# Performance work log

Hardware: AMD Instinct MI355X
Metric: run time of the kernel (lower is better)

## Reference

```python
import jax, jax.numpy as jnp
import numpy as np

HEADS = 12
DIM_HEAD = 64
SCALE = DIM_HEAD ** -0.5


def setup_inputs() -> dict:
    key = jax.random.key(0)
    k1, k2, k3 = jax.random.split(key, 3)
    B, N, D = 4, 2048, 768
    inner = HEADS * DIM_HEAD  # 768
    x = jax.random.normal(k1, (B, N, D), dtype=jnp.float32)
    W_qkv = jax.random.normal(k2, (D, 3 * inner), dtype=jnp.float32) * (D ** -0.5)
    W_out = jax.random.normal(k3, (inner, D), dtype=jnp.float32) * (inner ** -0.5)
    b_out = jnp.zeros((D,), dtype=jnp.float32)
    return {"x": x, "W_qkv": W_qkv, "W_out": W_out, "b_out": b_out}


def reference(x, W_qkv, W_out, b_out):
    B, N, D = x.shape
    qkv = x @ W_qkv  # [B, N, 3*inner]
    q, k, v = jnp.split(qkv, 3, axis=-1)
    # 'b n (h d) -> b h n d'
    def split_heads(t):
        return t.reshape(B, N, HEADS, DIM_HEAD).transpose(0, 2, 1, 3)
    q, k, v = split_heads(q), split_heads(k), split_heads(v)
    dots = jnp.einsum('bhnd,bhmd->bhnm', q, k) * SCALE  # [B, H, N, N]
    attn = jax.nn.softmax(dots, axis=-1)
    out = jnp.einsum('bhnm,bhmd->bhnd', attn, v)
    out = out.transpose(0, 2, 1, 3).reshape(B, N, HEADS * DIM_HEAD)  # 'b h n d -> b n (h d)'
    return out @ W_out + b_out
```

## Files before the change

kernel.cpp:

```cpp
#include <hip/hip_runtime.h>
#include <hip/hip_bf16.h>

typedef __bf16 bf16_t;
typedef __bf16 bf16x4 __attribute__((ext_vector_type(4)));
typedef __bf16 bf16x8 __attribute__((ext_vector_type(8)));
typedef float f32x4 __attribute__((ext_vector_type(4)));
typedef float f32x16 __attribute__((ext_vector_type(16)));
typedef unsigned int u32x4 __attribute__((ext_vector_type(4)));

#define HEADS 12
#define DHEAD 64
#define NSEQ 2048
#define BATCH 4
#define DMODEL 768
#define NINNER 768

#define QSCALE 0.18033688011112042f

__device__ __forceinline__ void gl_lds16(const bf16_t* g, bf16_t* l) {
  __builtin_amdgcn_global_load_lds(
      (const __attribute__((address_space(1))) void*)g,
      (__attribute__((address_space(3))) void*)l, 16, 0, 0);
}

__device__ __forceinline__ unsigned pack_bf16_2(float a, float b) {
  unsigned lo = (unsigned)__builtin_bit_cast(unsigned short, (bf16_t)a);
  unsigned hi = (unsigned)__builtin_bit_cast(unsigned short, (bf16_t)b);
  return lo | (hi << 16);
}

__global__ void cast_bf16_kernel(const float* __restrict__ in, bf16_t* __restrict__ out, int n8) {
  int i = blockIdx.x * blockDim.x + threadIdx.x;
  const int stride = gridDim.x * blockDim.x;
  for (; i < n8; i += stride) {
    const f32x4* p = (const f32x4*)(in + (size_t)i * 8);
    f32x4 a = p[0], b = p[1];
    bf16x8 o;
#pragma unroll
    for (int j = 0; j < 4; ++j) { o[j] = (bf16_t)a[j]; o[j + 4] = (bf16_t)b[j]; }
    *(bf16x8*)(out + (size_t)i * 8) = o;
  }
}

__global__ void transpose_cast_kernel(const float* __restrict__ in, bf16_t* __restrict__ out,
                                      int K, int N) {
  __shared__ float tile[32][33];
  const int bx = blockIdx.x * 32;
  const int by = blockIdx.y * 32;
  const int tx = threadIdx.x, ty = threadIdx.y;
#pragma unroll
  for (int i = ty; i < 32; i += 8)
    tile[i][tx] = in[(size_t)(by + i) * N + bx + tx];
  __syncthreads();
#pragma unroll
  for (int i = ty; i < 32; i += 8)
    out[(size_t)(bx + i) * K + by + tx] = (bf16_t)tile[tx][i];
}

template <int MODE>
__global__ __launch_bounds__(256, 2)
void gemm_bt(const bf16_t* __restrict__ A, const bf16_t* __restrict__ Bt,
             bf16_t* __restrict__ qw, bf16_t* __restrict__ kw, bf16_t* __restrict__ vtw,
             const float* __restrict__ bias, float* __restrict__ outf,
             int M, int Nn, int K) {
  __shared__ bf16_t As[128 * 64];
  __shared__ bf16_t Bs[128 * 64];
  const int tid = threadIdx.x;
  const int wid = tid >> 6;
  const int lane = tid & 63;
  const int m0 = blockIdx.x * 128;
  const int n0 = blockIdx.y * 128;
  const int arow = lane >> 3;
  const int acol = (lane & 7) * 8;
  const int wm = (wid >> 1) * 64;
  const int wn = (wid & 1) * 64;
  const int fr = lane & 15;
  const int fg = lane >> 4;

  f32x4 acc[4][4] = {};

  for (int kt = 0; kt < K; kt += 64) {
    __syncthreads();
#pragma unroll
    for (int i = 0; i < 4; ++i) {
      const int c = i * 4 + wid;
      gl_lds16(A + (size_t)(m0 + c * 8 + arow) * K + kt + acol, As + c * 512);
      gl_lds16(Bt + (size_t)(n0 + c * 8 + arow) * K + kt + acol, Bs + c * 512);
    }
    __syncthreads();
#pragma unroll
    for (int kk = 0; kk < 2; ++kk) {
      bf16x8 af[4], bfr[4];
#pragma unroll
      for (int mi = 0; mi < 4; ++mi)
        af[mi] = *(const bf16x8*)(As + (wm + mi * 16 + fr) * 64 + kk * 32 + fg * 8);
#pragma unroll
      for (int ni = 0; ni < 4; ++ni)
        bfr[ni] = *(const bf16x8*)(Bs + (wn + ni * 16 + fr) * 64 + kk * 32 + fg * 8);
#pragma unroll
      for (int mi = 0; mi < 4; ++mi)
#pragma unroll
        for (int ni = 0; ni < 4; ++ni)
          acc[mi][ni] = __builtin_amdgcn_mfma_f32_16x16x32_bf16(af[mi], bfr[ni], acc[mi][ni], 0, 0, 0);
    }
  }

  if (MODE == 0 && n0 >= 2 * NINNER) {
#pragma unroll
    for (int mi = 0; mi < 4; ++mi) {
#pragma unroll
      for (int ni = 0; ni < 4; ++ni) {
        const int col = n0 + wn + ni * 16 + fr - 2 * NINNER;
        const int h = col >> 6, d = col & 63;
        const int row0 = m0 + wm + mi * 16 + fg * 4;
        const int b = row0 >> 11, n = row0 & 2047;
        bf16x4 pk;
#pragma unroll
        for (int r = 0; r < 4; ++r) pk[r] = (bf16_t)acc[mi][ni][r];
        *(bf16x4*)(vtw + ((size_t)((b * HEADS + h) * DHEAD + d)) * NSEQ + n) = pk;
      }
    }
  } else {
#pragma unroll
    for (int mi = 0; mi < 4; ++mi) {
#pragma unroll
      for (int ni = 0; ni < 4; ++ni) {
#pragma unroll
        for (int r = 0; r < 4; ++r) {
          const int row = m0 + wm + mi * 16 + fg * 4 + r;
          const int col = n0 + wn + ni * 16 + fr;
          float val = acc[mi][ni][r];
          if (MODE == 0) {
            const int which = col / NINNER;
            const int cin = col - which * NINNER;
            const int h = cin >> 6, d = cin & 63;
            const int b = row >> 11, n = row & 2047;
            bf16_t* dst = (which == 0) ? qw : kw;
            if (which == 0) val *= QSCALE;
            dst[(((size_t)(b * HEADS + h)) * NSEQ + n) * DHEAD + d] = (bf16_t)val;
          } else {
            outf[(size_t)row * Nn + col] = val + bias[col];
          }
        }
      }
    }
  }
}

__global__ __launch_bounds__(256, 3)
void attn_fwd(const bf16_t* __restrict__ qg, const bf16_t* __restrict__ kg,
              const bf16_t* __restrict__ vtg, bf16_t* __restrict__ og) {
  __shared__ bf16_t KV[2][16 * 512];
  const int tid = threadIdx.x, wid = tid >> 6, lane = tid & 63;
  const int logical = (blockIdx.x & 7) * 96 + (blockIdx.x >> 3);
  const int bh = logical >> 4;
  const int qbase = (logical & 15) * 128 + wid * 32;
  const bf16_t* Q = qg + (size_t)bh * NSEQ * DHEAD;
  const bf16_t* K = kg + (size_t)bh * NSEQ * DHEAD;
  const bf16_t* Vt = vtg + (size_t)bh * NSEQ * DHEAD;
  const int l31 = lane & 31, hi = lane >> 5;
  const int sw = (l31 & 19) | ((l31 & 4) << 1) | ((l31 & 8) >> 1);

  bf16x8 qf[4];
#pragma unroll
  for (int ks = 0; ks < 4; ++ks)
    qf[ks] = *(const bf16x8*)(Q + (size_t)(qbase + l31) * DHEAD + ks * 16 + hi * 8);

  bf16x8 onesf;
#pragma unroll
  for (int e = 0; e < 8; ++e) onesf[e] = (bf16_t)1.0f;

  f32x16 oacc[2] = {};
  f32x16 lacc = {};

  auto stage = [&](int bsel, int t) {
    const int kv0 = t * 64;
#pragma unroll
    for (int i = 0; i < 4; ++i) {
      const int c = wid * 4 + i;
      bf16_t* dst = &KV[bsel][c * 512];
      if (c < 8) {
        gl_lds16(K + (size_t)(kv0 + (c >> 2) * 32 + sw) * DHEAD + (c & 3) * 16 + hi * 8, dst);
      } else {
        gl_lds16(Vt + (size_t)(((c >> 2) & 1) * 32 + l31) * NSEQ + kv0 + (c & 3) * 16 + hi * 8, dst);
      }
    }
  };

  stage(0, 0);

  for (int t = 0; t < NSEQ / 64; ++t) {
    const int buf = t & 1;
    asm volatile("s_waitcnt vmcnt(0) lgkmcnt(0)" ::: "memory");
    __builtin_amdgcn_sched_barrier(0);
    __syncthreads();
    if (t + 1 < NSEQ / 64) stage(buf ^ 1, t + 1);

    const bf16_t* base = &KV[buf][0];

    f32x16 sacc[2] = {};
    __builtin_amdgcn_s_setprio(1);
#pragma unroll
    for (int mi = 0; mi < 2; ++mi)
#pragma unroll
      for (int ks = 0; ks < 4; ++ks) {
        bf16x8 kf = *(const bf16x8*)(base + (mi * 4 + ks) * 512 + lane * 8);
        sacc[mi] = __builtin_amdgcn_mfma_f32_32x32x16_bf16(kf, qf[ks], sacc[mi], 0, 0, 0);
      }
    __builtin_amdgcn_s_setprio(0);

    bf16x8 pa[4];
#pragma unroll
    for (int mi = 0; mi < 2; ++mi) {
      float p[16];
#pragma unroll
      for (int r = 0; r < 16; ++r) p[r] = __builtin_amdgcn_exp2f(sacc[mi][r]);
#pragma unroll
      for (int s = 0; s < 2; ++s) {
        u32x4 pw;
#pragma unroll
        for (int w = 0; w < 4; ++w)
          pw[w] = pack_bf16_2(p[8 * s + 2 * w], p[8 * s + 2 * w + 1]);
        pa[mi * 2 + s] = __builtin_bit_cast(bf16x8, pw);
      }
    }

    __builtin_amdgcn_s_setprio(1);
#pragma unroll
    for (int ni = 0; ni < 2; ++ni)
#pragma unroll
      for (int ks = 0; ks < 4; ++ks) {
        bf16x8 vf = *(const bf16x8*)(base + (8 + ni * 4 + ks) * 512 + lane * 8);
        oacc[ni] = __builtin_amdgcn_mfma_f32_32x32x16_bf16(pa[ks], vf, oacc[ni], 0, 0, 0);
      }
#pragma unroll
    for (int ks = 0; ks < 4; ++ks)
      lacc = __builtin_amdgcn_mfma_f32_32x32x16_bf16(pa[ks], onesf, lacc, 0, 0, 0);
    __builtin_amdgcn_s_setprio(0);
  }

  const int b = bh / HEADS, h = bh % HEADS;
#pragma unroll
  for (int r = 0; r < 16; ++r) {
    const int qq = (r & 3) + 8 * (r >> 2) + 4 * hi;
    const float invr = 1.0f / lacc[r];
    const int n = qbase + qq;
#pragma unroll
    for (int ni = 0; ni < 2; ++ni)
      og[((size_t)b * NSEQ + n) * DMODEL + h * DHEAD + ni * 32 + l31] =
          (bf16_t)(oacc[ni][r] * invr);
  }
}

extern "C" void kernel_launch(void* const* d_in, const int* in_sizes, int n_in,
                              void* d_out, int out_size, void* d_ws, size_t ws_size,
                              hipStream_t stream) {
  const float* x    = (const float*)d_in[0];
  const float* Wqkv = (const float*)d_in[1];
  const float* Wout = (const float*)d_in[2];
  const float* bout = (const float*)d_in[3];
  float* out = (float*)d_out;

  char* ws = (char*)d_ws;
  bf16_t* xb    = (bf16_t*)(ws + 0);
  bf16_t* wqkvT = (bf16_t*)(ws + 12582912);
  bf16_t* woutT = (bf16_t*)(ws + 16121856);
  bf16_t* qw    = (bf16_t*)(ws + 17301504);
  bf16_t* kw    = (bf16_t*)(ws + 29884416);
  bf16_t* vtw   = (bf16_t*)(ws + 42467328);
  bf16_t* attno = (bf16_t*)(ws + 55050240);

  cast_bf16_kernel<<<1024, 256, 0, stream>>>(x, xb, (8192 * 768) / 8);
  transpose_cast_kernel<<<dim3(2304 / 32, 768 / 32), dim3(32, 8), 0, stream>>>(Wqkv, wqkvT, 768, 2304);
  transpose_cast_kernel<<<dim3(768 / 32, 768 / 32), dim3(32, 8), 0, stream>>>(Wout, woutT, 768, 768);

  gemm_bt<0><<<dim3(64, 18), 256, 0, stream>>>(xb, wqkvT, qw, kw, vtw, nullptr, nullptr,
                                               8192, 2304, 768);
  attn_fwd<<<768, 256, 0, stream>>>(qw, kw, vtw, attno);
  gemm_bt<1><<<dim3(64, 6), 256, 0, stream>>>(attno, woutT, nullptr, nullptr, nullptr, bout, out,
                                              8192, 768, 768);
}
```

Before: 151.6 us.

## Double-buffer GEMM LDS tiles and swizzle block order across XCDs

The GEMM kernels now use two LDS buffers, so the global-to-LDS load for the next K tile is issued before the MFMA work on the current tile. This is meant to hide load latency behind compute. The launch also changes to a 1D grid whose block index is remapped in groups of eight, spreading neighbouring tiles across XCDs for better L2 reuse. LDS use doubles to 64KB per block, which may limit occupancy. There is still a full wait and barrier on every iteration.

```diff
diff --git a/kernel.cpp b/kernel.cpp
--- a/kernel.cpp
+++ b/kernel.cpp
@@ -63,13 +63,16 @@
              bf16_t* __restrict__ qw, bf16_t* __restrict__ kw, bf16_t* __restrict__ vtw,
              const float* __restrict__ bias, float* __restrict__ outf,
              int M, int Nn, int K) {
-  __shared__ bf16_t As[128 * 64];
-  __shared__ bf16_t Bs[128 * 64];
+  __shared__ bf16_t As[2][128 * 64];
+  __shared__ bf16_t Bs[2][128 * 64];
   const int tid = threadIdx.x;
   const int wid = tid >> 6;
   const int lane = tid & 63;
-  const int m0 = blockIdx.x * 128;
-  const int n0 = blockIdx.y * 128;
+  const int q8 = gridDim.x >> 3;
+  const int swz = (blockIdx.x & 7) * q8 + (blockIdx.x >> 3);
+  const int nbm = M >> 7;
+  const int m0 = (swz % nbm) * 128;
+  const int n0 = (swz / nbm) * 128;
   const int arow = lane >> 3;
   const int acol = (lane & 7) * 8;
   const int wm = (wid >> 1) * 64;
@@ -79,24 +82,35 @@
 
   f32x4 acc[4][4] = {};
 
-  for (int kt = 0; kt < K; kt += 64) {
-    __syncthreads();
+  const int NT = K >> 6;
+  auto stageG = [&](int bsel, int t) {
+    const int kt = t * 64;
 #pragma unroll
     for (int i = 0; i < 4; ++i) {
       const int c = i * 4 + wid;
-      gl_lds16(A + (size_t)(m0 + c * 8 + arow) * K + kt + acol, As + c * 512);
-      gl_lds16(Bt + (size_t)(n0 + c * 8 + arow) * K + kt + acol, Bs + c * 512);
-    }
+      gl_lds16(A + (size_t)(m0 + c * 8 + arow) * K + kt + acol, &As[bsel][c * 512]);
+      gl_lds16(Bt + (size_t)(n0 + c * 8 + arow) * K + kt + acol, &Bs[bsel][c * 512]);
+    }
+  };
+
+  stageG(0, 0);
+
+  for (int t = 0; t < NT; ++t) {
+    const int buf = t & 1;
+    asm volatile("s_waitcnt vmcnt(0) lgkmcnt(0)" ::: "memory");
+    __builtin_amdgcn_sched_barrier(0);
     __syncthreads();
+    if (t + 1 < NT) stageG(buf ^ 1, t + 1);
+
 #pragma unroll
     for (int kk = 0; kk < 2; ++kk) {
       bf16x8 af[4], bfr[4];
 #pragma unroll
       for (int mi = 0; mi < 4; ++mi)
-        af[mi] = *(const bf16x8*)(As + (wm + mi * 16 + fr) * 64 + kk * 32 + fg * 8);
+        af[mi] = *(const bf16x8*)(&As[buf][(wm + mi * 16 + fr) * 64 + kk * 32 + fg * 8]);
 #pragma unroll
       for (int ni = 0; ni < 4; ++ni)
-        bfr[ni] = *(const bf16x8*)(Bs + (wn + ni * 16 + fr) * 64 + kk * 32 + fg * 8);
+        bfr[ni] = *(const bf16x8*)(&Bs[buf][(wn + ni * 16 + fr) * 64 + kk * 32 + fg * 8]);
 #pragma unroll
       for (int mi = 0; mi < 4; ++mi)
 #pragma unroll
@@ -274,9 +288,9 @@
   transpose_cast_kernel<<<dim3(2304 / 32, 768 / 32), dim3(32, 8), 0, stream>>>(Wqkv, wqkvT, 768, 2304);
   transpose_cast_kernel<<<dim3(768 / 32, 768 / 32), dim3(32, 8), 0, stream>>>(Wout, woutT, 768, 768);
 
-  gemm_bt<0><<<dim3(64, 18), 256, 0, stream>>>(xb, wqkvT, qw, kw, vtw, nullptr, nullptr,
-                                               8192, 2304, 768);
+  gemm_bt<0><<<1152, 256, 0, stream>>>(xb, wqkvT, qw, kw, vtw, nullptr, nullptr,
+                                       8192, 2304, 768);
   attn_fwd<<<768, 256, 0, stream>>>(qw, kw, vtw, attno);
-  gemm_bt<1><<<dim3(64, 6), 256, 0, stream>>>(attno, woutT, nullptr, nullptr, nullptr, bout, out,
-                                              8192, 768, 768);
-}
+  gemm_bt<1><<<384, 256, 0, stream>>>(attno, woutT, nullptr, nullptr, nullptr, bout, out,
+                                      8192, 768, 768);
+}
```

Result: slower. 170.8 us (+12.7%).

## Switch projection GEMM to 32x32x16 MFMA with fragment-ordered LDS layout

Applied to the files above, without the earlier changes.

The projection GEMM kernel now uses 32x32x16 bf16 MFMA instructions with 2x2 accumulators per wave instead of 16x16x32 with 4x4. Shared-memory tiles are stored in a fragment-native layout, so each lane reads its contiguous 16-byte operand directly, which is meant to avoid LDS bank conflicts from row-strided reads. Fewer, larger MFMAs and fewer LDS reads per k-step are intended to raise matrix-core throughput. Epilogue index math is rewritten for the 32x32 accumulator lane mapping, so any mapping error would produce wrong output.

```diff
diff --git a/kernel.cpp b/kernel.cpp
--- a/kernel.cpp
+++ b/kernel.cpp
@@ -63,72 +63,75 @@
              bf16_t* __restrict__ qw, bf16_t* __restrict__ kw, bf16_t* __restrict__ vtw,
              const float* __restrict__ bias, float* __restrict__ outf,
              int M, int Nn, int K) {
-  __shared__ bf16_t As[128 * 64];
-  __shared__ bf16_t Bs[128 * 64];
+  __shared__ bf16_t As[16 * 512];
+  __shared__ bf16_t Bs[16 * 512];
   const int tid = threadIdx.x;
   const int wid = tid >> 6;
   const int lane = tid & 63;
   const int m0 = blockIdx.x * 128;
   const int n0 = blockIdx.y * 128;
-  const int arow = lane >> 3;
-  const int acol = (lane & 7) * 8;
+  const int l31 = lane & 31, hi = lane >> 5;
   const int wm = (wid >> 1) * 64;
   const int wn = (wid & 1) * 64;
-  const int fr = lane & 15;
-  const int fg = lane >> 4;
-
-  f32x4 acc[4][4] = {};
+  const int mrb = (wid >> 1) * 2;
+  const int nrb = (wid & 1) * 2;
+
+  f32x16 acc[2][2] = {};
 
   for (int kt = 0; kt < K; kt += 64) {
     __syncthreads();
 #pragma unroll
     for (int i = 0; i < 4; ++i) {
-      const int c = i * 4 + wid;
-      gl_lds16(A + (size_t)(m0 + c * 8 + arow) * K + kt + acol, As + c * 512);
-      gl_lds16(Bt + (size_t)(n0 + c * 8 + arow) * K + kt + acol, Bs + c * 512);
+      gl_lds16(A + (size_t)(m0 + wid * 32 + l31) * K + kt + i * 16 + hi * 8,
+               As + (wid * 4 + i) * 512);
+      gl_lds16(Bt + (size_t)(n0 + wid * 32 + l31) * K + kt + i * 16 + hi * 8,
+               Bs + (wid * 4 + i) * 512);
     }
     __syncthreads();
 #pragma unroll
-    for (int kk = 0; kk < 2; ++kk) {
-      bf16x8 af[4], bfr[4];
-#pragma unroll
-      for (int mi = 0; mi < 4; ++mi)
-        af[mi] = *(const bf16x8*)(As + (wm + mi * 16 + fr) * 64 + kk * 32 + fg * 8);
-#pragma unroll
-      for (int ni = 0; ni < 4; ++ni)
-        bfr[ni] = *(const bf16x8*)(Bs + (wn + ni * 16 + fr) * 64 + kk * 32 + fg * 8);
-#pragma unroll
-      for (int mi = 0; mi < 4; ++mi)
-#pragma unroll
-        for (int ni = 0; ni < 4; ++ni)
-          acc[mi][ni] = __builtin_amdgcn_mfma_f32_16x16x32_bf16(af[mi], bfr[ni], acc[mi][ni], 0, 0, 0);
+    for (int ks = 0; ks < 4; ++ks) {
+      bf16x8 af[2], bfr[2];
+#pragma unroll
+      for (int mi = 0; mi < 2; ++mi)
+        af[mi] = *(const bf16x8*)(As + ((mrb + mi) * 4 + ks) * 512 + lane * 8);
+#pragma unroll
+      for (int ni = 0; ni < 2; ++ni)
+        bfr[ni] = *(const bf16x8*)(Bs + ((nrb + ni) * 4 + ks) * 512 + lane * 8);
+#pragma unroll
+      for (int mi = 0; mi < 2; ++mi)
+#pragma unroll
+        for (int ni = 0; ni < 2; ++ni)
+          acc[mi][ni] = __builtin_amdgcn_mfma_f32_32x32x16_bf16(af[mi], bfr[ni], acc[mi][ni], 0, 0, 0);
     }
   }
 
   if (MODE == 0 && n0 >= 2 * NINNER) {
 #pragma unroll
-    for (int mi = 0; mi < 4; ++mi) {
-#pragma unroll
-      for (int ni = 0; ni < 4; ++ni) {
-        const int col = n0 + wn + ni * 16 + fr - 2 * NINNER;
+    for (int mi = 0; mi < 2; ++mi) {
+#pragma unroll
+      for (int ni = 0; ni < 2; ++ni) {
+        const int col = n0 + wn + ni * 32 + l31 - 2 * NINNER;
         const int h = col >> 6, d = col & 63;
-        const int row0 = m0 + wm + mi * 16 + fg * 4;
-        const int b = row0 >> 11, n = row0 & 2047;
-        bf16x4 pk;
-#pragma unroll
-        for (int r = 0; r < 4; ++r) pk[r] = (bf16_t)acc[mi][ni][r];
-        *(bf16x4*)(vtw + ((size_t)((b * HEADS + h) * DHEAD + d)) * NSEQ + n) = pk;
+#pragma unroll
+        for (int q4 = 0; q4 < 4; ++q4) {
+          const int row0 = m0 + wm + mi * 32 + q4 * 8 + hi * 4;
+          const int b = row0 >> 11, n = row0 & 2047;
+          bf16x4 pk;
+#pragma unroll
+          for (int r = 0; r < 4; ++r) pk[r] = (bf16_t)acc[mi][ni][q4 * 4 + r];
+          *(bf16x4*)(vtw + ((size_t)((b * HEADS + h) * DHEAD + d)) * NSEQ + n) = pk;
+        }
       }
     }
   } else {
 #pragma unroll
-    for (int mi = 0; mi < 4; ++mi) {
-#pragma unroll
-      for (int ni = 0; ni < 4; ++ni) {
-#pragma unroll
-        for (int r = 0; r < 4; ++r) {
-          const int row = m0 + wm + mi * 16 + fg * 4 + r;
-          const int col = n0 + wn + ni * 16 + fr;
+    for (int mi = 0; mi < 2; ++mi) {
+#pragma unroll
+      for (int ni = 0; ni < 2; ++ni) {
+        const int col = n0 + wn + ni * 32 + l31;
+#pragma unroll
+        for (int r = 0; r < 16; ++r) {
+          const int row = m0 + wm + mi * 32 + (r & 3) + 8 * (r >> 2) + 4 * hi;
           float val = acc[mi][ni][r];
           if (MODE == 0) {
             const int which = col / NINNER;
```

New measurement: 184.0 us. 1.21x slower.

## Merge prologue cast kernels and double-buffer GEMM LDS tiles with prefetch

Applied to the files above, without the earlier changes.

The three preprocessing kernels (x cast and the two weight transpose-casts) are merged into one launch that dispatches on block index, cutting launch overhead. The GEMM now uses two 32-wide K buffers in LDS: the next tile is issued via global_load_lds while MFMAs consume the current one, with one barrier per iteration instead of two. K-steps are halved in size, so there are twice as many iterations and synchronisation points.

```diff
diff --git a/kernel.cpp b/kernel.cpp
--- a/kernel.cpp
+++ b/kernel.cpp
@@ -29,32 +29,49 @@
   return lo | (hi << 16);
 }
 
-__global__ void cast_bf16_kernel(const float* __restrict__ in, bf16_t* __restrict__ out, int n8) {
-  int i = blockIdx.x * blockDim.x + threadIdx.x;
-  const int stride = gridDim.x * blockDim.x;
-  for (; i < n8; i += stride) {
-    const f32x4* p = (const f32x4*)(in + (size_t)i * 8);
-    f32x4 a = p[0], b = p[1];
-    bf16x8 o;
-#pragma unroll
-    for (int j = 0; j < 4; ++j) { o[j] = (bf16_t)a[j]; o[j + 4] = (bf16_t)b[j]; }
-    *(bf16x8*)(out + (size_t)i * 8) = o;
-  }
-}
-
-__global__ void transpose_cast_kernel(const float* __restrict__ in, bf16_t* __restrict__ out,
-                                      int K, int N) {
+__global__ void prologue_kernel(const float* __restrict__ x,
+                                const float* __restrict__ Wqkv,
+                                const float* __restrict__ Wout,
+                                bf16_t* __restrict__ xb,
+                                bf16_t* __restrict__ wqkvT,
+                                bf16_t* __restrict__ woutT) {
   __shared__ float tile[32][33];
-  const int bx = blockIdx.x * 32;
-  const int by = blockIdx.y * 32;
-  const int tx = threadIdx.x, ty = threadIdx.y;
-#pragma unroll
-  for (int i = ty; i < 32; i += 8)
-    tile[i][tx] = in[(size_t)(by + i) * N + bx + tx];
-  __syncthreads();
-#pragma unroll
-  for (int i = ty; i < 32; i += 8)
-    out[(size_t)(bx + i) * K + by + tx] = (bf16_t)tile[tx][i];
+  const int bid = blockIdx.x;
+  const int tid = threadIdx.x;
+  if (bid < 384) {
+    const int n8 = (8192 * 768) / 8;
+    int i = bid * 256 + tid;
+    const int stride = 384 * 256;
+    for (; i < n8; i += stride) {
+      const f32x4* p = (const f32x4*)(x + (size_t)i * 8);
+      f32x4 a = p[0], b = p[1];
+      bf16x8 o;
+#pragma unroll
+      for (int j = 0; j < 4; ++j) { o[j] = (bf16_t)a[j]; o[j + 4] = (bf16_t)b[j]; }
+      *(bf16x8*)(xb + (size_t)i * 8) = o;
+    }
+  } else {
+    const float* in;
+    bf16_t* out;
+    int K, N, bx, by;
+    if (bid < 2112) {
+      const int tt = bid - 384;
+      in = Wqkv; out = wqkvT; K = 768; N = 2304;
+      bx = (tt % 72) * 32; by = (tt / 72) * 32;
+    } else {
+      const int tt = bid - 2112;
+      in = Wout; out = woutT; K = 768; N = 768;
+      bx = (tt % 24) * 32; by = (tt / 24) * 32;
+    }
+    const int tx = tid & 31, ty = tid >> 5;
+#pragma unroll
+    for (int i = ty; i < 32; i += 8)
+      tile[i][tx] = in[(size_t)(by + i) * N + bx + tx];
+    __syncthreads();
+#pragma unroll
+    for (int i = ty; i < 32; i += 8)
+      out[(size_t)(bx + i) * K + by + tx] = (bf16_t)tile[tx][i];
+  }
 }
 
 template <int MODE>
@@ -63,46 +80,54 @@
              bf16_t* __restrict__ qw, bf16_t* __restrict__ kw, bf16_t* __restrict__ vtw,
              const float* __restrict__ bias, float* __restrict__ outf,
              int M, int Nn, int K) {
-  __shared__ bf16_t As[128 * 64];
-  __shared__ bf16_t Bs[128 * 64];
+  __shared__ bf16_t As[2][128 * 32];
+  __shared__ bf16_t Bs[2][128 * 32];
   const int tid = threadIdx.x;
   const int wid = tid >> 6;
   const int lane = tid & 63;
   const int m0 = blockIdx.x * 128;
   const int n0 = blockIdx.y * 128;
-  const int arow = lane >> 3;
-  const int acol = (lane & 7) * 8;
   const int wm = (wid >> 1) * 64;
   const int wn = (wid & 1) * 64;
   const int fr = lane & 15;
   const int fg = lane >> 4;
+  const int srow = lane >> 2;
+  const int scol = (lane & 3) * 8;
 
   f32x4 acc[4][4] = {};
 
-  for (int kt = 0; kt < K; kt += 64) {
+  const int NT = K >> 5;
+  auto stageG = [&](int bsel, int t) {
+    const int kt = t * 32;
+#pragma unroll
+    for (int i = 0; i < 2; ++i) {
+      const int c = wid * 2 + i;
+      gl_lds16(A + (size_t)(m0 + c * 16 + srow) * K + kt + scol, &As[bsel][c * 512]);
+      gl_lds16(Bt + (size_t)(n0 + c * 16 + srow) * K + kt + scol, &Bs[bsel][c * 512]);
+    }
+  };
+
+  stageG(0, 0);
+
+  for (int t = 0; t < NT; ++t) {
+    const int buf = t & 1;
+    asm volatile("s_waitcnt vmcnt(0) lgkmcnt(0)" ::: "memory");
+    __builtin_amdgcn_sched_barrier(0);
     __syncthreads();
-#pragma unroll
-    for (int i = 0; i < 4; ++i) {
-      const int c = i * 4 + wid;
-      gl_lds16(A + (size_t)(m0 + c * 8 + arow) * K + kt + acol, As + c * 512);
-      gl_lds16(Bt + (size_t)(n0 + c * 8 + arow) * K + kt + acol, Bs + c * 512);
-    }
-    __syncthreads();
-#pragma unroll
-    for (int kk = 0; kk < 2; ++kk) {
-      bf16x8 af[4], bfr[4];
-#pragma unroll
-      for (int mi = 0; mi < 4; ++mi)
-        af[mi] = *(const bf16x8*)(As + (wm + mi * 16 + fr) * 64 + kk * 32 + fg * 8);
+    if (t + 1 < NT) stageG(buf ^ 1, t + 1);
+
+    bf16x8 af[4], bfr[4];
+#pragma unroll
+    for (int mi = 0; mi < 4; ++mi)
+      af[mi] = *(const bf16x8*)(&As[buf][(wm + mi * 16 + fr) * 32 + fg * 8]);
+#pragma unroll
+    for (int ni = 0; ni < 4; ++ni)
+      bfr[ni] = *(const bf16x8*)(&Bs[buf][(wn + ni * 16 + fr) * 32 + fg * 8]);
+#pragma unroll
+    for (int mi = 0; mi < 4; ++mi)
 #pragma unroll
       for (int ni = 0; ni < 4; ++ni)
-        bfr[ni] = *(const bf16x8*)(Bs + (wn + ni * 16 + fr) * 64 + kk * 32 + fg * 8);
-#pragma unroll
-      for (int mi = 0; mi < 4; ++mi)
-#pragma unroll
-        for (int ni = 0; ni < 4; ++ni)
-          acc[mi][ni] = __builtin_amdgcn_mfma_f32_16x16x32_bf16(af[mi], bfr[ni], acc[mi][ni], 0, 0, 0);
-    }
+        acc[mi][ni] = __builtin_amdgcn_mfma_f32_16x16x32_bf16(af[mi], bfr[ni], acc[mi][ni], 0, 0, 0);
   }
 
   if (MODE == 0 && n0 >= 2 * NINNER) {
@@ -270,9 +295,7 @@
   bf16_t* vtw   = (bf16_t*)(ws + 42467328);
   bf16_t* attno = (bf16_t*)(ws + 55050240);
 
-  cast_bf16_kernel<<<1024, 256, 0, stream>>>(x, xb, (8192 * 768) / 8);
-  transpose_cast_kernel<<<dim3(2304 / 32, 768 / 32), dim3(32, 8), 0, stream>>>(Wqkv, wqkvT, 768, 2304);
-  transpose_cast_kernel<<<dim3(768 / 32, 768 / 32), dim3(32, 8), 0, stream>>>(Wout, woutT, 768, 768);
+  prologue_kernel<<<2688, 256, 0, stream>>>(x, Wqkv, Wout, xb, wqkvT, woutT);
 
   gemm_bt<0><<<dim3(64, 18), 256, 0, stream>>>(xb, wqkvT, qw, kw, vtw, nullptr, nullptr,
                                                8192, 2304, 768);
```

New measurement: 151.9 us. Within noise of the previous version (+0.2%).
